# Optimization experiments

Hardware: AMD Instinct MI355X
Metric: run time of the kernel (lower is better)

The kernel has to match this reference:

```python
import jax, jax.numpy as jnp
import numpy as np

B, S, D0, H, K, C = 128, 64, 768, 256, 7, 3
EPS = 1e-12


def setup_inputs() -> dict:
    key = jax.random.key(0)
    ks = jax.random.split(key, 8)
    return {
        "premise": jax.random.normal(ks[0], (B, S, D0), jnp.float32),
        "hypothesis": jax.random.normal(ks[1], (B, S, D0), jnp.float32),
        "aW1": jax.random.normal(ks[2], (S, D0), jnp.float32) * 0.02,
        "conv1_w": jax.random.normal(ks[3], (D0, K, 2, H), jnp.float32) * 0.02,
        "conv1_b": jnp.full((H,), 1e-4, jnp.float32),
        "aW2": jax.random.normal(ks[4], (S, H), jnp.float32) * 0.02,
        "conv2_w": jax.random.normal(ks[5], (H, K, 2, H), jnp.float32) * 0.02,
        "conv2_b": jnp.full((H,), 1e-4, jnp.float32),
        "out_w": jax.random.normal(ks[6], (3, C), jnp.float32) * 0.1,
        "out_b": jnp.zeros((C,), jnp.float32),
    }


def _att_mat(x1, x2):
    # x1, x2: [B, d, W]; euclidean pairwise-distance attention 1/(1+||x1_i - x2_j||)
    n1 = jnp.sum(x1 * x1, axis=1)                       # [B, W]
    n2 = jnp.sum(x2 * x2, axis=1)                       # [B, W]
    dot = jnp.einsum('bdi,bdj->bij', x1, x2)            # [B, W, W]
    sq = jnp.maximum(n1[:, :, None] + n2[:, None, :] - 2.0 * dot, 0.0)
    return 1.0 / (1.0 + jnp.sqrt(sq + EPS))


def _cos_sim(v1, v2):
    n1 = jnp.sqrt(jnp.sum(v1 * v1, axis=1))
    n2 = jnp.sqrt(jnp.sum(v2 * v2, axis=1))
    return jnp.sum(v1 * v2, axis=1) / (n1 * n2 + EPS)


def _cnn_layer(x1, x2, aW, cw, cb):
    # x1, x2: [B, d, S]; aW: [S, d]; cw: [d, K, 2, H] (HWIO); cb: [H]
    att = _att_mat(x1, x2)                              # [B, S, S]
    # x1_a = (att @ aW)^T, x2_a = (att^T @ aW)^T  ->  [B, d, S]
    x1a = jnp.einsum('bij,jd->bdi', att, aW)
    x2a = jnp.einsum('bji,jd->bdi', att, aW)

    def conv(x, xa):
        xin = jnp.stack([x, xa], axis=-1)               # [B, d, S, 2] NHWC
        xin = jnp.pad(xin, ((0, 0), (0, 0), (K - 1, K - 1), (0, 0)))
        y = jax.lax.conv_general_dilated(
            xin, cw, window_strides=(1, 1), padding='VALID',
            dimension_numbers=('NHWC', 'HWIO', 'NHWC'))  # [B, 1, S+K-1, H]
        return jnp.transpose(jnp.tanh(y + cb)[:, 0], (0, 2, 1))  # [B, H, S+K-1]

    lc = conv(x1, x1a)
    rc = conv(x2, x2a)

    att2 = _att_mat(lc, rc)                             # [B, S+K-1, S+K-1]
    la = jnp.sum(att2, axis=2)                          # [B, S+K-1]
    ra = jnp.sum(att2, axis=1)                          # [B, S+K-1]

    def w_pool(x, a):
        # attention-weighted sliding-window sum of width K -> [B, H, S]
        w = x * a[:, None, :]
        return sum(w[:, :, j:j + S] for j in range(K))

    lwp = w_pool(lc, la)
    rwp = w_pool(rc, ra)
    lap = jnp.mean(lc, axis=2)                          # all-pool -> [B, H]
    rap = jnp.mean(rc, axis=2)
    return lwp, lap, rwp, rap


def _forward(premise, hypothesis, aW1, conv1_w, conv1_b, aW2, conv2_w, conv2_b,
             out_w, out_b):
    x1 = jnp.transpose(premise, (0, 2, 1))              # [B, D0, S]
    x2 = jnp.transpose(hypothesis, (0, 2, 1))
    LO0 = jnp.mean(x1, axis=2)                          # [B, D0]
    RO0 = jnp.mean(x2, axis=2)
    LI1, LO1, RI1, RO1 = _cnn_layer(x1, x2, aW1, conv1_w, conv1_b)
    _, LO2, _, RO2 = _cnn_layer(LI1, RI1, aW2, conv2_w, conv2_b)
    sims = jnp.stack(
        [_cos_sim(LO0, RO0), _cos_sim(LO1, RO1), _cos_sim(LO2, RO2)], axis=1)
    return sims @ out_w + out_b                         # logits [B, C]


def reference(premise, hypothesis, aW1, conv1_w, conv1_b, aW2, conv2_w,
              conv2_b, out_w, out_b):
    return _forward(premise, hypothesis, aW1, conv1_w, conv1_b, aW2, conv2_w,
                    conv2_b, out_w, out_b)
```

## Files before the change

### kernel.cpp

```cpp
#include <hip/hip_runtime.h>
#include <math.h>

typedef _Float16 f16;
typedef _Float16 half8 __attribute__((ext_vector_type(8)));
typedef _Float16 half4 __attribute__((ext_vector_type(4)));
typedef float floatx4 __attribute__((ext_vector_type(4)));

constexpr int B   = 128;
constexpr int S   = 64;
constexpr int D0  = 768;
constexpr int H   = 256;
constexpr int KW  = 7;
constexpr int NC  = 3;
constexpr int T70 = S + KW - 1;
constexpr float EPSF = 1e-12f;

__device__ __forceinline__ void gload16(const void* g, void* l) {
  __builtin_amdgcn_global_load_lds(
      (const __attribute__((address_space(1))) unsigned int*)g,
      (__attribute__((address_space(3))) unsigned int*)l, 16, 0, 0);
}

__global__ __launch_bounds__(256) void k_cvtmean(const float* __restrict__ in0,
                                                 const float* __restrict__ in1,
                                                 f16* __restrict__ oh0,
                                                 f16* __restrict__ oh1,
                                                 float* __restrict__ mn0,
                                                 float* __restrict__ mn1) {
  constexpr int D4 = D0 / 4;
  const int side = blockIdx.y;
  const float* __restrict__ in = side ? in1 : in0;
  f16* __restrict__ outh = side ? oh1 : oh0;
  float* __restrict__ mean = side ? mn1 : mn0;
  const int idx = blockIdx.x * 256 + threadIdx.x;
  const int b = idx / D4, f4 = idx % D4;
  const float4* __restrict__ src = reinterpret_cast<const float4*>(in) + (size_t)b * S * D4 + f4;
  half4* __restrict__ dst = reinterpret_cast<half4*>(outh) + (size_t)b * S * D4 + f4;
  float4 acc = {0.f, 0.f, 0.f, 0.f};
  for (int t = 0; t < S; ++t) {
    float4 v = src[(size_t)t * D4];
    acc.x += v.x; acc.y += v.y; acc.z += v.z; acc.w += v.w;
    half4 o = {(f16)v.x, (f16)v.y, (f16)v.z, (f16)v.w};
    dst[(size_t)t * D4] = o;
  }
  const float inv = 1.f / S;
  mean[(size_t)b * D0 + f4 * 4 + 0] = acc.x * inv;
  mean[(size_t)b * D0 + f4 * 4 + 1] = acc.y * inv;
  mean[(size_t)b * D0 + f4 * 4 + 2] = acc.z * inv;
  mean[(size_t)b * D0 + f4 * 4 + 3] = acc.w * inv;
}

__global__ __launch_bounds__(256) void k_trw_x(const float* __restrict__ cw,
                                               f16* __restrict__ Weff, int DPC, int Ktot) {
  __shared__ f16 tile[64][65];
  const int k = blockIdx.z;
  const int dd0 = blockIdx.x * 64, h0 = blockIdx.y * 64;
  const int tx = threadIdx.x & 63, ty = threadIdx.x >> 6;
#pragma unroll
  for (int i = 0; i < 64; i += 4) {
    int dd = dd0 + i + ty;
    tile[i + ty][tx] = (f16)cw[(size_t)((dd * KW + k) * 2 + 0) * H + h0 + tx];
  }
  __syncthreads();
  const int sbase = ((dd0 >> 6) * 7 + k) * 64;
#pragma unroll
  for (int i = 0; i < 64; i += 4) {
    int h = h0 + i + ty;
    int col = sbase + (((tx >> 3) ^ (h & 7)) << 3) + (tx & 7);
    Weff[(size_t)h * Ktot + col] = tile[tx][i + ty];
  }
}

template<int D>
__global__ __launch_bounds__(256) void k_vgemm(const float* __restrict__ aW,
                                               const float* __restrict__ cw,
                                               f16* __restrict__ Weff) {
  constexpr int NX7 = (D / 64) * 7;
  constexpr int KTOT = (NX7 + 7) * 64;
  __shared__ half8 As[64 * 4];
  __shared__ half8 Bs[64 * 4];
  const int kk = blockIdx.x;
  const int h0 = blockIdx.y * 64;
  const int tid = threadIdx.x;
  const int lane = tid & 63, wave = tid >> 6;
  const int wr = wave >> 1, wc = wave & 1;
  const int l15 = lane & 15, g = lane >> 4;

  floatx4 acc[2][2];
#pragma unroll
  for (int i = 0; i < 2; ++i)
#pragma unroll
    for (int j = 0; j < 2; ++j) acc[i][j] = (floatx4)0.f;

  for (int k0 = 0; k0 < D; k0 += 32) {
    __syncthreads();
    {
      const int r = tid >> 2, cch = tid & 3;
      const float4* s = reinterpret_cast<const float4*>(aW + (size_t)r * D + k0 + cch * 8);
      float4 v0 = s[0], v1 = s[1];
      half8 hv = {(f16)v0.x, (f16)v0.y, (f16)v0.z, (f16)v0.w,
                  (f16)v1.x, (f16)v1.y, (f16)v1.z, (f16)v1.w};
      As[r * 4 + (cch ^ ((r >> 1) & 3))] = hv;
      const int hrow = tid & 63, kc = tid >> 6;
      half8 bv;
#pragma unroll
      for (int e = 0; e < 8; ++e) {
        const int d = k0 + kc * 8 + e;
        bv[e] = (f16)cw[(size_t)((d * KW + kk) * 2 + 1) * H + h0 + hrow];
      }
      Bs[hrow * 4 + (kc ^ ((hrow >> 1) & 3))] = bv;
    }
    __syncthreads();
    half8 af[2], bf[2];
#pragma unroll
    for (int fi = 0; fi < 2; ++fi) {
      const int row = wr * 32 + fi * 16 + l15;
      af[fi] = As[row * 4 + (g ^ ((row >> 1) & 3))];
    }
#pragma unroll
    for (int fj = 0; fj < 2; ++fj) {
      const int row = wc * 32 + fj * 16 + l15;
      bf[fj] = Bs[row * 4 + (g ^ ((row >> 1) & 3))];
    }
#pragma unroll
    for (int fi = 0; fi < 2; ++fi)
#pragma unroll
      for (int fj = 0; fj < 2; ++fj)
        acc[fi][fj] = __builtin_amdgcn_mfma_f32_16x16x32_f16(af[fi], bf[fj], acc[fi][fj], 0, 0, 0);
  }
  const int base = (NX7 + kk) * 64;
#pragma unroll
  for (int fi = 0; fi < 2; ++fi)
#pragma unroll
    for (int fj = 0; fj < 2; ++fj)
#pragma unroll
      for (int r = 0; r < 4; ++r) {
        const int j = wr * 32 + fi * 16 + g * 4 + r;
        const int h = h0 + wc * 32 + fj * 16 + l15;
        const int col = base + (((j >> 3) ^ (h & 7)) << 3) + (j & 7);
        Weff[(size_t)h * KTOT + col] = (f16)acc[fi][fj][r];
      }
}

__global__ __launch_bounds__(256) void k_mean2(const f16* __restrict__ xa,
                                               const f16* __restrict__ xb,
                                               float* __restrict__ oa,
                                               float* __restrict__ ob) {
  const int side = blockIdx.y;
  const f16* __restrict__ x = side ? xb : xa;
  float* __restrict__ o = side ? ob : oa;
  int idx = blockIdx.x * 256 + threadIdx.x;
  if (idx >= B * H) return;
  int b = idx / H, f = idx % H;
  const f16* p = x + (size_t)b * T70 * H + f;
  float s = 0.f;
  for (int t = 0; t < T70; ++t) s += (float)p[(size_t)t * H];
  o[idx] = s * (1.f / T70);
}

template<int W, int WP, int D, bool SUMS>
__global__ __launch_bounds__(256) void k_att(const f16* __restrict__ X1,
                                             const f16* __restrict__ X2,
                                             float* __restrict__ la,
                                             float* __restrict__ ra) {
  constexpr int FR = WP / 32;
  __shared__ half8 As[WP * 4];
  __shared__ half8 Bs[WP * 4];
  __shared__ float n1s[WP], n2s[WP];
  __shared__ float att_s[SUMS ? WP * (WP + 1) : 1];

  const int b = blockIdx.x, tid = threadIdx.x;
  const int lane = tid & 63, wave = tid >> 6;
  const int wr = wave >> 1, wc = wave & 1;
  const int l15 = lane & 15, g = lane >> 4;
  const f16* __restrict__ x1 = X1 + (size_t)b * W * D;
  const f16* __restrict__ x2 = X2 + (size_t)b * W * D;

  floatx4 acc[FR][FR];
#pragma unroll
  for (int i = 0; i < FR; ++i)
#pragma unroll
    for (int j = 0; j < FR; ++j) acc[i][j] = (floatx4)0.f;
  float na1 = 0.f, na2 = 0.f;

  for (int k0 = 0; k0 < D; k0 += 32) {
    __syncthreads();
    for (int u = tid; u < WP * 4; u += 256) {
      const int r = u >> 2, c = u & 3;
      half8 v1 = (half8)(f16)0.f, v2 = (half8)(f16)0.f;
      if (r < W) {
        v1 = *reinterpret_cast<const half8*>(x1 + (size_t)r * D + k0 + c * 8);
        v2 = *reinterpret_cast<const half8*>(x2 + (size_t)r * D + k0 + c * 8);
      }
      const int p = r * 4 + (c ^ ((r >> 1) & 3));
      As[p] = v1;
      Bs[p] = v2;
    }
    __syncthreads();
    half8 af[FR], bf[FR];
#pragma unroll
    for (int fi = 0; fi < FR; ++fi) {
      const int row = wr * 16 * FR + fi * 16 + l15;
      af[fi] = As[row * 4 + (g ^ ((row >> 1) & 3))];
    }
#pragma unroll
    for (int fj = 0; fj < FR; ++fj) {
      const int row = wc * 16 * FR + fj * 16 + l15;
      bf[fj] = Bs[row * 4 + (g ^ ((row >> 1) & 3))];
    }
#pragma unroll
    for (int fi = 0; fi < FR; ++fi)
#pragma unroll
      for (int fj = 0; fj < FR; ++fj)
        acc[fi][fj] = __builtin_amdgcn_mfma_f32_16x16x32_f16(af[fi], bf[fj], acc[fi][fj], 0, 0, 0);
    if (tid < WP) {
      const int r = tid;
#pragma unroll
      for (int c = 0; c < 4; ++c) {
        half8 v = As[r * 4 + (c ^ ((r >> 1) & 3))];
#pragma unroll
        for (int e = 0; e < 8; ++e) { float f = (float)v[e]; na1 = fmaf(f, f, na1); }
      }
    } else if (tid >= 128 && tid < 128 + WP) {
      const int r = tid - 128;
#pragma unroll
      for (int c = 0; c < 4; ++c) {
        half8 v = Bs[r * 4 + (c ^ ((r >> 1) & 3))];
#pragma unroll
        for (int e = 0; e < 8; ++e) { float f = (float)v[e]; na2 = fmaf(f, f, na2); }
      }
    }
  }
  if (tid < WP) n1s[tid] = na1;
  if (tid >= 128 && tid < 128 + WP) n2s[tid - 128] = na2;
  __syncthreads();

#pragma unroll
  for (int fi = 0; fi < FR; ++fi)
#pragma unroll
    for (int fj = 0; fj < FR; ++fj)
#pragma unroll
      for (int r = 0; r < 4; ++r) {
        const int i = wr * 16 * FR + fi * 16 + g * 4 + r;
        const int j = wc * 16 * FR + fj * 16 + l15;
        if (i < W && j < W) {
          float sq = fmaxf(n1s[i] + n2s[j] - 2.f * acc[fi][fj][r], 0.f);
          const float v = 1.f / (1.f + sqrtf(sq + EPSF));
          if (SUMS) att_s[i * (WP + 1) + j] = v;
        }
      }
  if (SUMS) {
    __syncthreads();
    if (tid < W) {
      float sum = 0.f;
      for (int j = 0; j < W; ++j) sum += att_s[tid * (WP + 1) + j];
      la[b * W + tid] = sum;
    }
    if (tid >= 128 && tid < 128 + W) {
      const int j = tid - 128;
      float sum = 0.f;
      for (int i = 0; i < W; ++i) sum += att_s[i * (WP + 1) + j];
      ra[b * W + j] = sum;
    }
  }
}

template<int D>
__global__ __launch_bounds__(256) void k_attst(const f16* __restrict__ X1,
                                               const f16* __restrict__ X2,
                                               f16* __restrict__ attA,
                                               f16* __restrict__ attT) {
  __shared__ half8 As[64 * 4];
  __shared__ half8 Bs[64 * 4];
  __shared__ float n1s[64], n2s[64];
  __shared__ half8 atA[64 * 8];
  __shared__ half8 atT[64 * 8];

  const int b = blockIdx.x, tid = threadIdx.x;
  const int lane = tid & 63, wave = tid >> 6;
  const int wr = wave >> 1, wc = wave & 1;
  const int l15 = lane & 15, g = lane >> 4;
  const f16* __restrict__ x1 = X1 + (size_t)b * S * D;
  const f16* __restrict__ x2 = X2 + (size_t)b * S * D;

  floatx4 acc[2][2];
#pragma unroll
  for (int i = 0; i < 2; ++i)
#pragma unroll
    for (int j = 0; j < 2; ++j) acc[i][j] = (floatx4)0.f;
  float na1 = 0.f, na2 = 0.f;

  for (int k0 = 0; k0 < D; k0 += 32) {
    __syncthreads();
    {
      const int r = tid >> 2, c = tid & 3;
      const int p = r * 4 + (c ^ ((r >> 1) & 3));
      As[p] = *reinterpret_cast<const half8*>(x1 + (size_t)r * D + k0 + c * 8);
      Bs[p] = *reinterpret_cast<const half8*>(x2 + (size_t)r * D + k0 + c * 8);
    }
    __syncthreads();
    half8 af[2], bf[2];
#pragma unroll
    for (int fi = 0; fi < 2; ++fi) {
      const int row = wr * 32 + fi * 16 + l15;
      af[fi] = As[row * 4 + (g ^ ((row >> 1) & 3))];
    }
#pragma unroll
    for (int fj = 0; fj < 2; ++fj) {
      const int row = wc * 32 + fj * 16 + l15;
      bf[fj] = Bs[row * 4 + (g ^ ((row >> 1) & 3))];
    }
#pragma unroll
    for (int fi = 0; fi < 2; ++fi)
#pragma unroll
      for (int fj = 0; fj < 2; ++fj)
        acc[fi][fj] = __builtin_amdgcn_mfma_f32_16x16x32_f16(af[fi], bf[fj], acc[fi][fj], 0, 0, 0);
    if (tid < 64) {
      const int r = tid;
#pragma unroll
      for (int c = 0; c < 4; ++c) {
        half8 v = As[r * 4 + (c ^ ((r >> 1) & 3))];
#pragma unroll
        for (int e = 0; e < 8; ++e) { float f = (float)v[e]; na1 = fmaf(f, f, na1); }
      }
    } else if (tid >= 128 && tid < 192) {
      const int r = tid - 128;
#pragma unroll
      for (int c = 0; c < 4; ++c) {
        half8 v = Bs[r * 4 + (c ^ ((r >> 1) & 3))];
#pragma unroll
        for (int e = 0; e < 8; ++e) { float f = (float)v[e]; na2 = fmaf(f, f, na2); }
      }
    }
  }
  if (tid < 64) n1s[tid] = na1;
  if (tid >= 128 && tid < 192) n2s[tid - 128] = na2;
  __syncthreads();

  f16* atAe = reinterpret_cast<f16*>(atA);
  f16* atTe = reinterpret_cast<f16*>(atT);
#pragma unroll
  for (int fi = 0; fi < 2; ++fi)
#pragma unroll
    for (int fj = 0; fj < 2; ++fj)
#pragma unroll
      for (int r = 0; r < 4; ++r) {
        const int i = wr * 32 + fi * 16 + g * 4 + r;
        const int j = wc * 32 + fj * 16 + l15;
        float sq = fmaxf(n1s[i] + n2s[j] - 2.f * acc[fi][fj][r], 0.f);
        const f16 v = (f16)(1.f / (1.f + sqrtf(sq + EPSF)));
        atAe[(i * 8 + ((j >> 3) ^ (i & 7))) * 8 + (j & 7)] = v;
        atTe[(j * 8 + ((i >> 3) ^ (j & 7))) * 8 + (i & 7)] = v;
      }
  __syncthreads();
  half8* Ag = reinterpret_cast<half8*>(attA) + (size_t)b * 512;
  half8* Tg = reinterpret_cast<half8*>(attT) + (size_t)b * 512;
  for (int idx = tid; idx < 512; idx += 256) {
    const int i = idx >> 3, ch = idx & 7;
    Ag[idx] = atA[i * 8 + (ch ^ (i & 7))];
    Tg[idx] = atT[i * 8 + (ch ^ (i & 7))];
  }
}

template<int DPC>
__global__ __launch_bounds__(256) void k_conv(const f16* __restrict__ X0,
                                              const f16* __restrict__ X1v,
                                              const f16* __restrict__ At0,
                                              const f16* __restrict__ At1,
                                              const f16* __restrict__ Weff,
                                              const float* __restrict__ bias,
                                              f16* __restrict__ O16_0,
                                              f16* __restrict__ O16_1) {
  constexpr int NDQX = DPC / 64;
  constexpr int NX7 = NDQX * 7;
  constexpr int NSTEP = NX7 + 7;
  constexpr int KTOT = NSTEP * 64;
  __shared__ half8 Wl[70 * 8];
  __shared__ half8 B8[2][128 * 8];

  const int tid = threadIdx.x;
  const int bid = blockIdx.x;
  const int xcd = bid & 7, slot = bid >> 3;
  const int n0 = (xcd >> 2) * 128;
  const int w = slot * 4 + (xcd & 3);
  const int z = w & 1, mblk = w >> 1;
  const int m0 = mblk * 64;
  const f16* __restrict__ Xs  = z ? X1v : X0;
  const f16* __restrict__ Ats = z ? At1 : At0;
  f16* __restrict__ Out16 = z ? O16_1 : O16_0;

  const int lane = tid & 63, wave = tid >> 6;
  const int wr = wave >> 1, wc = wave & 1;
  const int l15 = lane & 15, g = lane >> 4;
  const int r0 = tid >> 3, c8 = tid & 7;

  int jr[3] = {r0, r0 + 32, 64 + r0};
  int aoffX[3], aoffA[3];
  bool aval[3];
#pragma unroll
  for (int p = 0; p < 3; ++p) {
    const int u = m0 - 6 + jr[p];
    const int uc = u < 0 ? 0 : u;
    const int bn = uc / T70;
    const int tl = uc - bn * T70;
    aval[p] = (u >= 0) && (tl < S);
    aoffX[p] = (bn * S + tl) * DPC + c8 * 8;
    aoffA[p] = (bn * 64 + tl) * 64 + c8 * 8;
  }
  const bool has2 = (r0 < 6);
  const int bchunk0 = wave * 64 + lane;
  const f16* __restrict__ bsrc = Weff + (size_t)n0 * KTOT;

  floatx4 acc[2][4];
#pragma unroll
  for (int i = 0; i < 2; ++i)
#pragma unroll
    for (int j = 0; j < 4; ++j) acc[i][j] = (floatx4)0.f;

  half8 rA[3];
  auto aLoad = [&](const f16* __restrict__ src, const int* aoff, int co) {
#pragma unroll
    for (int p = 0; p < 2; ++p)
      rA[p] = aval[p] ? *reinterpret_cast<const half8*>(src + aoff[p] + co)
                      : (half8)(f16)0.f;
    if (has2)
      rA[2] = aval[2] ? *reinterpret_cast<const half8*>(src + aoff[2] + co)
                      : (half8)(f16)0.f;
  };
  auto aWrite = [&]() {
#pragma unroll
    for (int p = 0; p < 2; ++p) {
      const int j = jr[p];
      Wl[j * 8 + (c8 ^ (j & 7))] = rA[p];
    }
    if (has2) {
      const int j = jr[2];
      Wl[j * 8 + (c8 ^ (j & 7))] = rA[2];
    }
  };
  auto bStage = [&](int buf, int ks) {
    const int o = ks * 64;
#pragma unroll
    for (int q = 0; q < 4; ++q) {
      const int chunk = q * 256 + bchunk0;
      const int r = chunk >> 3, cc = chunk & 7;
      gload16(bsrc + (size_t)r * KTOT + o + cc * 8, &B8[buf][q * 256 + wave * 64]);
    }
  };
  auto compute = [&](int ks) {
    const int k = (ks < NX7) ? (ks % 7) : (ks - NX7);
    const int buf = ks & 1;
    half8 af[2][2], bf[4][2];
#pragma unroll
    for (int i = 0; i < 2; ++i) {
      const int j = wr * 32 + i * 16 + l15 + k;
#pragma unroll
      for (int s = 0; s < 2; ++s)
        af[i][s] = Wl[j * 8 + ((s * 4 + g) ^ (j & 7))];
    }
#pragma unroll
    for (int jx = 0; jx < 4; ++jx) {
      const int row = wc * 64 + jx * 16 + l15;
#pragma unroll
      for (int s = 0; s < 2; ++s)
        bf[jx][s] = B8[buf][row * 8 + ((s * 4 + g) ^ (row & 7))];
    }
#pragma unroll
    for (int s = 0; s < 2; ++s)
#pragma unroll
      for (int i = 0; i < 2; ++i)
#pragma unroll
        for (int jx = 0; jx < 4; ++jx)
          acc[i][jx] = __builtin_amdgcn_mfma_f32_16x16x32_f16(af[i][s], bf[jx][s], acc[i][jx], 0, 0, 0);
  };

  bStage(0, 0);
  aLoad(Xs, aoffX, 0);
  aWrite();
  __syncthreads();

  for (int ks = 0; ks < NSTEP; ++ks) {
    const int nxt = ks + 1;
    const bool more = nxt < NSTEP;
    if (more) {
      bStage(nxt & 1, nxt);
      if (ks % 7 == 5) {
        const int wnd = ks / 7 + 1;
        if (wnd < NDQX) aLoad(Xs, aoffX, wnd * 64);
        else if (wnd == NDQX) aLoad(Ats, aoffA, 0);
      }
    }
    compute(ks);
    if (more && (nxt % 7 == 0)) { __syncthreads(); aWrite(); }
    __syncthreads();
  }

#pragma unroll
  for (int i = 0; i < 2; ++i) {
    const int mr = m0 + wr * 32 + i * 16 + g * 4;
#pragma unroll
    for (int jx = 0; jx < 4; ++jx) {
      const int h = n0 + wc * 64 + jx * 16 + l15;
      const float bv = bias[h];
#pragma unroll
      for (int r = 0; r < 4; ++r)
        Out16[(size_t)(mr + r) * H + h] = (f16)tanhf(acc[i][jx][r] + bv);
    }
  }
}

__global__ __launch_bounds__(256) void k_powl(const f16* __restrict__ lcTh,
                                              const f16* __restrict__ rcTh,
                                              const float* __restrict__ la,
                                              const float* __restrict__ ra,
                                              float* __restrict__ LO1,
                                              float* __restrict__ RO1,
                                              f16* __restrict__ LI1h,
                                              f16* __restrict__ RI1h) {
  const int b = blockIdx.x, side = blockIdx.y;
  const f16* __restrict__ xc = (side ? rcTh : lcTh) + (size_t)b * T70 * H;
  const float* __restrict__ av = (side ? ra : la) + (size_t)b * T70;
  float* __restrict__ LO = side ? RO1 : LO1;
  f16* __restrict__ LI = (side ? RI1h : LI1h) + (size_t)b * S * H;
  __shared__ float a_s[T70];
  __shared__ f16 wv[T70][H];
  const int h = threadIdx.x;
  if (h < T70) a_s[h] = av[h];
  __syncthreads();
  float sum = 0.f;
  for (int t = 0; t < T70; ++t) {
    const float v = (float)xc[(size_t)t * H + h];
    sum += v;
    wv[t][h] = (f16)(v * a_s[t]);
  }
  LO[(size_t)b * H + h] = sum * (1.f / T70);
  __syncthreads();
  for (int s = 0; s < S; ++s) {
    float acc = 0.f;
#pragma unroll
    for (int j = 0; j < KW; ++j) acc += (float)wv[s + j][h];
    LI[(size_t)s * H + h] = (f16)acc;
  }
}

__global__ __launch_bounds__(256) void k_final(const float* __restrict__ LO0,
                                               const float* __restrict__ RO0,
                                               const float* __restrict__ LO1,
                                               const float* __restrict__ RO1,
                                               const float* __restrict__ LO2,
                                               const float* __restrict__ RO2,
                                               const float* __restrict__ out_w,
                                               const float* __restrict__ out_b,
                                               float* __restrict__ out) {
  const int b = blockIdx.x;
  const int tid = threadIdx.x;
  __shared__ float red[3][4];
  __shared__ float sims[3];
  const float* Ls[3] = {LO0 + (size_t)b * D0, LO1 + (size_t)b * H, LO2 + (size_t)b * H};
  const float* Rs[3] = {RO0 + (size_t)b * D0, RO1 + (size_t)b * H, RO2 + (size_t)b * H};
  const int dims[3] = {D0, H, H};
#pragma unroll
  for (int p = 0; p < 3; ++p) {
    float dot = 0.f, q1 = 0.f, q2 = 0.f;
    for (int i = tid; i < dims[p]; i += 256) {
      const float v1 = Ls[p][i], v2 = Rs[p][i];
      dot = fmaf(v1, v2, dot);
      q1  = fmaf(v1, v1, q1);
      q2  = fmaf(v2, v2, q2);
    }
#pragma unroll
    for (int off = 32; off > 0; off >>= 1) {
      dot += __shfl_down(dot, off);
      q1  += __shfl_down(q1, off);
      q2  += __shfl_down(q2, off);
    }
    if ((tid & 63) == 0) { red[0][tid >> 6] = dot; red[1][tid >> 6] = q1; red[2][tid >> 6] = q2; }
    __syncthreads();
    if (tid == 0) {
      float d = red[0][0] + red[0][1] + red[0][2] + red[0][3];
      float a = red[1][0] + red[1][1] + red[1][2] + red[1][3];
      float c = red[2][0] + red[2][1] + red[2][2] + red[2][3];
      sims[p] = d / (sqrtf(a) * sqrtf(c) + EPSF);
    }
    __syncthreads();
  }
  if (tid < NC) {
    float v = out_b[tid];
#pragma unroll
    for (int k = 0; k < 3; ++k) v = fmaf(sims[k], out_w[k * NC + tid], v);
    out[b * NC + tid] = v;
  }
}

extern "C" void kernel_launch(void* const* d_in, const int* in_sizes, int n_in,
                              void* d_out, int out_size, void* d_ws, size_t ws_size,
                              hipStream_t stream) {
  const float* premise    = (const float*)d_in[0];
  const float* hypothesis = (const float*)d_in[1];
  const float* aW1        = (const float*)d_in[2];
  const float* conv1_w    = (const float*)d_in[3];
  const float* conv1_b    = (const float*)d_in[4];
  const float* aW2        = (const float*)d_in[5];
  const float* conv2_w    = (const float*)d_in[6];
  const float* conv2_b    = (const float*)d_in[7];
  const float* out_w      = (const float*)d_in[8];
  const float* out_b      = (const float*)d_in[9];
  float* out = (float*)d_out;

  constexpr int KTOT1 = ((D0 / 64) * 7 + 7) * 64;
  constexpr int KTOT2 = ((H  / 64) * 7 + 7) * 64;

  char* ws = (char*)d_ws;
  size_t off = 0;
  auto alloc = [&](size_t bytes) {
    void* p = ws + off;
    off += (bytes + 255) & ~(size_t)255;
    return p;
  };
  f16*   Weff1 = (f16*)alloc((size_t)H * KTOT1 * 2);
  f16*   Weff2 = (f16*)alloc((size_t)H * KTOT2 * 2);
  f16*   Xh    = (f16*)alloc((size_t)B * S * D0 * 2);
  f16*   Yh    = (f16*)alloc((size_t)B * S * D0 * 2);
  f16*   attA  = (f16*)alloc((size_t)B * S * S * 2);
  f16*   attT  = (f16*)alloc((size_t)B * S * S * 2);
  f16*   LI1h  = (f16*)alloc((size_t)B * S * H * 2);
  f16*   RI1h  = (f16*)alloc((size_t)B * S * H * 2);
  f16*   lcTh  = (f16*)alloc((size_t)B * T70 * H * 2);
  f16*   rcTh  = (f16*)alloc((size_t)B * T70 * H * 2);
  float* LO0   = (float*)alloc((size_t)B * D0 * 4);
  float* RO0   = (float*)alloc((size_t)B * D0 * 4);
  float* LO1   = (float*)alloc((size_t)B * H * 4);
  float* RO1   = (float*)alloc((size_t)B * H * 4);
  float* LO2   = (float*)alloc((size_t)B * H * 4);
  float* RO2   = (float*)alloc((size_t)B * H * 4);
  float* la    = (float*)alloc((size_t)B * T70 * 4);
  float* ra    = (float*)alloc((size_t)B * T70 * 4);

  k_cvtmean<<<dim3(B * (D0 / 4) / 256, 2), 256, 0, stream>>>(premise, hypothesis, Xh, Yh, LO0, RO0);
  k_trw_x<<<dim3(D0 / 64, H / 64, 7), 256, 0, stream>>>(conv1_w, Weff1, D0, KTOT1);
  k_trw_x<<<dim3(H / 64,  H / 64, 7), 256, 0, stream>>>(conv2_w, Weff2, H, KTOT2);
  k_vgemm<D0><<<dim3(7, H / 64), 256, 0, stream>>>(aW1, conv1_w, Weff1);
  k_vgemm<H ><<<dim3(7, H / 64), 256, 0, stream>>>(aW2, conv2_w, Weff2);
  k_attst<D0><<<B, 256, 0, stream>>>(Xh, Yh, attA, attT);
  k_conv<D0><<<560, 256, 0, stream>>>(Xh, Yh, attA, attT, Weff1, conv1_b, lcTh, rcTh);
  k_att<T70, 96, H, true><<<B, 256, 0, stream>>>(lcTh, rcTh, la, ra);
  k_powl<<<dim3(B, 2), 256, 0, stream>>>(lcTh, rcTh, la, ra, LO1, RO1, LI1h, RI1h);
  k_attst<H><<<B, 256, 0, stream>>>(LI1h, RI1h, attA, attT);
  k_conv<H><<<560, 256, 0, stream>>>(LI1h, RI1h, attA, attT, Weff2, conv2_b, lcTh, rcTh);
  k_mean2<<<dim3((B * H + 255) / 256, 2), 256, 0, stream>>>(lcTh, rcTh, LO2, RO2);
  k_final<<<B, 256, 0, stream>>>(LO0, RO0, LO1, RO1, LO2, RO2, out_w, out_b, out);
}
```

Before: 226.2 us.

## Fuse weight-prep and pooling kernels, triple-buffer conv pipeline with raw barriers

The four weight-preparation launches become one kernel, k_wprep, that picks its role from the block index. The attention-sum and weighted-pool kernels are merged into k_pool, one block per batch that handles both sides. The final mean of the second layer's conv outputs moves into k_final. The conv GEMM now triple-buffers the B operand and double-buffers the A window, and uses explicit vmcnt waits, s_barrier and setprio around the MFMAs instead of __syncthreads. This cuts launch count and intermediate round trips, and overlaps loads with MFMA work. The cost is more LDS per conv block, hand-tuned wait counts that could be fragile, and k_pool running half as many blocks as the old pooling kernel.

```diff
diff --git a/kernel.cpp b/kernel.cpp
--- a/kernel.cpp
+++ b/kernel.cpp
@@ -14,6 +14,8 @@
 constexpr int NC  = 3;
 constexpr int T70 = S + KW - 1;
 constexpr float EPSF = 1e-12f;
+constexpr int KTOT1 = ((D0 / 64) * 7 + 7) * 64;
+constexpr int KTOT2 = ((H  / 64) * 7 + 7) * 64;
 
 __device__ __forceinline__ void gload16(const void* g, void* l) {
   __builtin_amdgcn_global_load_lds(
@@ -50,11 +52,14 @@
   mean[(size_t)b * D0 + f4 * 4 + 3] = acc.w * inv;
 }
 
-__global__ __launch_bounds__(256) void k_trw_x(const float* __restrict__ cw,
-                                               f16* __restrict__ Weff, int DPC, int Ktot) {
-  __shared__ f16 tile[64][65];
-  const int k = blockIdx.z;
-  const int dd0 = blockIdx.x * 64, h0 = blockIdx.y * 64;
+__device__ __forceinline__ void trw_x_dev(const float* __restrict__ cw,
+                                          f16* __restrict__ Weff,
+                                          int DPC, int Ktot, int t,
+                                          f16 (*tile)[65]) {
+  const int nb = DPC / 64;
+  const int k = t / (nb * 4);
+  const int rem = t % (nb * 4);
+  const int h0 = (rem / nb) * 64, dd0 = (rem % nb) * 64;
   const int tx = threadIdx.x & 63, ty = threadIdx.x >> 6;
 #pragma unroll
   for (int i = 0; i < 64; i += 4) {
@@ -71,16 +76,13 @@
   }
 }
 
-template<int D>
-__global__ __launch_bounds__(256) void k_vgemm(const float* __restrict__ aW,
-                                               const float* __restrict__ cw,
-                                               f16* __restrict__ Weff) {
-  constexpr int NX7 = (D / 64) * 7;
-  constexpr int KTOT = (NX7 + 7) * 64;
-  __shared__ half8 As[64 * 4];
-  __shared__ half8 Bs[64 * 4];
-  const int kk = blockIdx.x;
-  const int h0 = blockIdx.y * 64;
+__device__ __forceinline__ void vgemm_dev(const float* __restrict__ aW,
+                                          const float* __restrict__ cw,
+                                          f16* __restrict__ Weff,
+                                          int D, int Ktot, int t,
+                                          half8* As, half8* Bs) {
+  const int kk = t % 7;
+  const int h0 = (t / 7) * 64;
   const int tid = threadIdx.x;
   const int lane = tid & 63, wave = tid >> 6;
   const int wr = wave >> 1, wc = wave & 1;
@@ -128,7 +130,7 @@
       for (int fj = 0; fj < 2; ++fj)
         acc[fi][fj] = __builtin_amdgcn_mfma_f32_16x16x32_f16(af[fi], bf[fj], acc[fi][fj], 0, 0, 0);
   }
-  const int base = (NX7 + kk) * 64;
+  const int base = ((D / 64) * 7 + kk) * 64;
 #pragma unroll
   for (int fi = 0; fi < 2; ++fi)
 #pragma unroll
@@ -138,131 +140,24 @@
         const int j = wr * 32 + fi * 16 + g * 4 + r;
         const int h = h0 + wc * 32 + fj * 16 + l15;
         const int col = base + (((j >> 3) ^ (h & 7)) << 3) + (j & 7);
-        Weff[(size_t)h * KTOT + col] = (f16)acc[fi][fj][r];
-      }
-}
-
-__global__ __launch_bounds__(256) void k_mean2(const f16* __restrict__ xa,
-                                               const f16* __restrict__ xb,
-                                               float* __restrict__ oa,
-                                               float* __restrict__ ob) {
-  const int side = blockIdx.y;
-  const f16* __restrict__ x = side ? xb : xa;
-  float* __restrict__ o = side ? ob : oa;
-  int idx = blockIdx.x * 256 + threadIdx.x;
-  if (idx >= B * H) return;
-  int b = idx / H, f = idx % H;
-  const f16* p = x + (size_t)b * T70 * H + f;
-  float s = 0.f;
-  for (int t = 0; t < T70; ++t) s += (float)p[(size_t)t * H];
-  o[idx] = s * (1.f / T70);
-}
-
-template<int W, int WP, int D, bool SUMS>
-__global__ __launch_bounds__(256) void k_att(const f16* __restrict__ X1,
-                                             const f16* __restrict__ X2,
-                                             float* __restrict__ la,
-                                             float* __restrict__ ra) {
-  constexpr int FR = WP / 32;
-  __shared__ half8 As[WP * 4];
-  __shared__ half8 Bs[WP * 4];
-  __shared__ float n1s[WP], n2s[WP];
-  __shared__ float att_s[SUMS ? WP * (WP + 1) : 1];
-
-  const int b = blockIdx.x, tid = threadIdx.x;
-  const int lane = tid & 63, wave = tid >> 6;
-  const int wr = wave >> 1, wc = wave & 1;
-  const int l15 = lane & 15, g = lane >> 4;
-  const f16* __restrict__ x1 = X1 + (size_t)b * W * D;
-  const f16* __restrict__ x2 = X2 + (size_t)b * W * D;
-
-  floatx4 acc[FR][FR];
-#pragma unroll
-  for (int i = 0; i < FR; ++i)
-#pragma unroll
-    for (int j = 0; j < FR; ++j) acc[i][j] = (floatx4)0.f;
-  float na1 = 0.f, na2 = 0.f;
-
-  for (int k0 = 0; k0 < D; k0 += 32) {
-    __syncthreads();
-    for (int u = tid; u < WP * 4; u += 256) {
-      const int r = u >> 2, c = u & 3;
-      half8 v1 = (half8)(f16)0.f, v2 = (half8)(f16)0.f;
-      if (r < W) {
-        v1 = *reinterpret_cast<const half8*>(x1 + (size_t)r * D + k0 + c * 8);
-        v2 = *reinterpret_cast<const half8*>(x2 + (size_t)r * D + k0 + c * 8);
-      }
-      const int p = r * 4 + (c ^ ((r >> 1) & 3));
-      As[p] = v1;
-      Bs[p] = v2;
-    }
-    __syncthreads();
-    half8 af[FR], bf[FR];
-#pragma unroll
-    for (int fi = 0; fi < FR; ++fi) {
-      const int row = wr * 16 * FR + fi * 16 + l15;
-      af[fi] = As[row * 4 + (g ^ ((row >> 1) & 3))];
-    }
-#pragma unroll
-    for (int fj = 0; fj < FR; ++fj) {
-      const int row = wc * 16 * FR + fj * 16 + l15;
-      bf[fj] = Bs[row * 4 + (g ^ ((row >> 1) & 3))];
-    }
-#pragma unroll
-    for (int fi = 0; fi < FR; ++fi)
-#pragma unroll
-      for (int fj = 0; fj < FR; ++fj)
-        acc[fi][fj] = __builtin_amdgcn_mfma_f32_16x16x32_f16(af[fi], bf[fj], acc[fi][fj], 0, 0, 0);
-    if (tid < WP) {
-      const int r = tid;
-#pragma unroll
-      for (int c = 0; c < 4; ++c) {
-        half8 v = As[r * 4 + (c ^ ((r >> 1) & 3))];
-#pragma unroll
-        for (int e = 0; e < 8; ++e) { float f = (float)v[e]; na1 = fmaf(f, f, na1); }
-      }
-    } else if (tid >= 128 && tid < 128 + WP) {
-      const int r = tid - 128;
-#pragma unroll
-      for (int c = 0; c < 4; ++c) {
-        half8 v = Bs[r * 4 + (c ^ ((r >> 1) & 3))];
-#pragma unroll
-        for (int e = 0; e < 8; ++e) { float f = (float)v[e]; na2 = fmaf(f, f, na2); }
-      }
-    }
-  }
-  if (tid < WP) n1s[tid] = na1;
-  if (tid >= 128 && tid < 128 + WP) n2s[tid - 128] = na2;
-  __syncthreads();
-
-#pragma unroll
-  for (int fi = 0; fi < FR; ++fi)
-#pragma unroll
-    for (int fj = 0; fj < FR; ++fj)
-#pragma unroll
-      for (int r = 0; r < 4; ++r) {
-        const int i = wr * 16 * FR + fi * 16 + g * 4 + r;
-        const int j = wc * 16 * FR + fj * 16 + l15;
-        if (i < W && j < W) {
-          float sq = fmaxf(n1s[i] + n2s[j] - 2.f * acc[fi][fj][r], 0.f);
-          const float v = 1.f / (1.f + sqrtf(sq + EPSF));
-          if (SUMS) att_s[i * (WP + 1) + j] = v;
-        }
-      }
-  if (SUMS) {
-    __syncthreads();
-    if (tid < W) {
-      float sum = 0.f;
-      for (int j = 0; j < W; ++j) sum += att_s[tid * (WP + 1) + j];
-      la[b * W + tid] = sum;
-    }
-    if (tid >= 128 && tid < 128 + W) {
-      const int j = tid - 128;
-      float sum = 0.f;
-      for (int i = 0; i < W; ++i) sum += att_s[i * (WP + 1) + j];
-      ra[b * W + j] = sum;
-    }
-  }
+        Weff[(size_t)h * Ktot + col] = (f16)acc[fi][fj][r];
+      }
+}
+
+__global__ __launch_bounds__(256) void k_wprep(const float* __restrict__ cw1,
+                                               const float* __restrict__ aW1,
+                                               f16* __restrict__ Weff1,
+                                               const float* __restrict__ cw2,
+                                               const float* __restrict__ aW2,
+                                               f16* __restrict__ Weff2) {
+  __shared__ f16 tile[64][65];
+  __shared__ half8 As[64 * 4];
+  __shared__ half8 Bs[64 * 4];
+  const int bid = blockIdx.x;
+  if (bid < 336)        trw_x_dev(cw1, Weff1, D0, KTOT1, bid, tile);
+  else if (bid < 364)   vgemm_dev(aW1, cw1, Weff1, D0, KTOT1, bid - 336, As, Bs);
+  else if (bid < 476)   trw_x_dev(cw2, Weff2, H, KTOT2, bid - 364, tile);
+  else                  vgemm_dev(aW2, cw2, Weff2, H, KTOT2, bid - 476, As, Bs);
 }
 
 template<int D>
@@ -375,8 +270,8 @@
   constexpr int NX7 = NDQX * 7;
   constexpr int NSTEP = NX7 + 7;
   constexpr int KTOT = NSTEP * 64;
-  __shared__ half8 Wl[70 * 8];
-  __shared__ half8 B8[2][128 * 8];
+  __shared__ half8 Wl[2][70 * 8];
+  __shared__ half8 B8[3][128 * 8];
 
   const int tid = threadIdx.x;
   const int bid = blockIdx.x;
@@ -427,15 +322,15 @@
       rA[2] = aval[2] ? *reinterpret_cast<const half8*>(src + aoff[2] + co)
                       : (half8)(f16)0.f;
   };
-  auto aWrite = [&]() {
+  auto aWrite = [&](int bufA) {
 #pragma unroll
     for (int p = 0; p < 2; ++p) {
       const int j = jr[p];
-      Wl[j * 8 + (c8 ^ (j & 7))] = rA[p];
+      Wl[bufA][j * 8 + (c8 ^ (j & 7))] = rA[p];
     }
     if (has2) {
       const int j = jr[2];
-      Wl[j * 8 + (c8 ^ (j & 7))] = rA[2];
+      Wl[bufA][j * 8 + (c8 ^ (j & 7))] = rA[2];
     }
   };
   auto bStage = [&](int buf, int ks) {
@@ -448,15 +343,16 @@
     }
   };
   auto compute = [&](int ks) {
-    const int k = (ks < NX7) ? (ks % 7) : (ks - NX7);
-    const int buf = ks & 1;
+    const int k = ks % 7;
+    const int buf = ks % 3;
+    const int bufA = (ks / 7) & 1;
     half8 af[2][2], bf[4][2];
 #pragma unroll
     for (int i = 0; i < 2; ++i) {
       const int j = wr * 32 + i * 16 + l15 + k;
 #pragma unroll
       for (int s = 0; s < 2; ++s)
-        af[i][s] = Wl[j * 8 + ((s * 4 + g) ^ (j & 7))];
+        af[i][s] = Wl[bufA][j * 8 + ((s * 4 + g) ^ (j & 7))];
     }
 #pragma unroll
     for (int jx = 0; jx < 4; ++jx) {
@@ -465,6 +361,7 @@
       for (int s = 0; s < 2; ++s)
         bf[jx][s] = B8[buf][row * 8 + ((s * 4 + g) ^ (row & 7))];
     }
+    __builtin_amdgcn_s_setprio(1);
 #pragma unroll
     for (int s = 0; s < 2; ++s)
 #pragma unroll
@@ -472,27 +369,38 @@
 #pragma unroll
         for (int jx = 0; jx < 4; ++jx)
           acc[i][jx] = __builtin_amdgcn_mfma_f32_16x16x32_f16(af[i][s], bf[jx][s], acc[i][jx], 0, 0, 0);
+    __builtin_amdgcn_s_setprio(0);
   };
 
   bStage(0, 0);
   aLoad(Xs, aoffX, 0);
-  aWrite();
-  __syncthreads();
+  bStage(1, 1);
+  aWrite(0);
+  asm volatile("s_waitcnt vmcnt(4) lgkmcnt(0)" ::: "memory");
+  __builtin_amdgcn_s_barrier();
+  __builtin_amdgcn_sched_barrier(0);
 
   for (int ks = 0; ks < NSTEP; ++ks) {
-    const int nxt = ks + 1;
-    const bool more = nxt < NSTEP;
-    if (more) {
-      bStage(nxt & 1, nxt);
-      if (ks % 7 == 5) {
-        const int wnd = ks / 7 + 1;
-        if (wnd < NDQX) aLoad(Xs, aoffX, wnd * 64);
-        else if (wnd == NDQX) aLoad(Ats, aoffA, 0);
-      }
+    const int nxt = ks + 1, nn = ks + 2;
+    if (nn < NSTEP) bStage(nn % 3, nn);
+    if ((ks % 7) == 5) {
+      const int wnd = ks / 7 + 1;
+      if (wnd < NDQX) aLoad(Xs, aoffX, wnd * 64);
+      else if (wnd == NDQX) aLoad(Ats, aoffA, 0);
     }
     compute(ks);
-    if (more && (nxt % 7 == 0)) { __syncthreads(); aWrite(); }
-    __syncthreads();
+    const bool awr = (nxt < NSTEP) && ((nxt % 7) == 0);
+    if (awr) aWrite((nxt / 7) & 1);
+    if (nxt < NSTEP) {
+      if (nn < NSTEP) {
+        if (awr) asm volatile("s_waitcnt vmcnt(4) lgkmcnt(0)" ::: "memory");
+        else     asm volatile("s_waitcnt vmcnt(4)" ::: "memory");
+      } else {
+        asm volatile("s_waitcnt vmcnt(0) lgkmcnt(0)" ::: "memory");
+      }
+      __builtin_amdgcn_s_barrier();
+      __builtin_amdgcn_sched_barrier(0);
+    }
   }
 
 #pragma unroll
@@ -509,37 +417,136 @@
   }
 }
 
-__global__ __launch_bounds__(256) void k_powl(const f16* __restrict__ lcTh,
+__global__ __launch_bounds__(256) void k_pool(const f16* __restrict__ lcTh,
                                               const f16* __restrict__ rcTh,
-                                              const float* __restrict__ la,
-                                              const float* __restrict__ ra,
                                               float* __restrict__ LO1,
                                               float* __restrict__ RO1,
                                               f16* __restrict__ LI1h,
                                               f16* __restrict__ RI1h) {
-  const int b = blockIdx.x, side = blockIdx.y;
-  const f16* __restrict__ xc = (side ? rcTh : lcTh) + (size_t)b * T70 * H;
-  const float* __restrict__ av = (side ? ra : la) + (size_t)b * T70;
-  float* __restrict__ LO = side ? RO1 : LO1;
-  f16* __restrict__ LI = (side ? RI1h : LI1h) + (size_t)b * S * H;
-  __shared__ float a_s[T70];
-  __shared__ f16 wv[T70][H];
-  const int h = threadIdx.x;
-  if (h < T70) a_s[h] = av[h];
+  constexpr int W = T70, WP = 96, D = H;
+  constexpr int FR = WP / 32;
+  __shared__ half8 As[WP * 4];
+  __shared__ half8 Bs[WP * 4];
+  __shared__ float n1s[WP], n2s[WP];
+  __shared__ float att_s[WP * (WP + 1)];
+  __shared__ float la_s[W], ra_s[W];
+
+  const int b = blockIdx.x, tid = threadIdx.x;
+  const int lane = tid & 63, wave = tid >> 6;
+  const int wr = wave >> 1, wc = wave & 1;
+  const int l15 = lane & 15, g = lane >> 4;
+  const f16* __restrict__ x1 = lcTh + (size_t)b * W * D;
+  const f16* __restrict__ x2 = rcTh + (size_t)b * W * D;
+
+  floatx4 acc[FR][FR];
+#pragma unroll
+  for (int i = 0; i < FR; ++i)
+#pragma unroll
+    for (int j = 0; j < FR; ++j) acc[i][j] = (floatx4)0.f;
+  float na1 = 0.f, na2 = 0.f;
+
+  for (int k0 = 0; k0 < D; k0 += 32) {
+    __syncthreads();
+    for (int u = tid; u < WP * 4; u += 256) {
+      const int r = u >> 2, c = u & 3;
+      half8 v1 = (half8)(f16)0.f, v2 = (half8)(f16)0.f;
+      if (r < W) {
+        v1 = *reinterpret_cast<const half8*>(x1 + (size_t)r * D + k0 + c * 8);
+        v2 = *reinterpret_cast<const half8*>(x2 + (size_t)r * D + k0 + c * 8);
+      }
+      const int p = r * 4 + (c ^ ((r >> 1) & 3));
+      As[p] = v1;
+      Bs[p] = v2;
+    }
+    __syncthreads();
+    half8 af[FR], bf[FR];
+#pragma unroll
+    for (int fi = 0; fi < FR; ++fi) {
+      const int row = wr * 16 * FR + fi * 16 + l15;
+      af[fi] = As[row * 4 + (g ^ ((row >> 1) & 3))];
+    }
+#pragma unroll
+    for (int fj = 0; fj < FR; ++fj) {
+      const int row = wc * 16 * FR + fj * 16 + l15;
+      bf[fj] = Bs[row * 4 + (g ^ ((row >> 1) & 3))];
+    }
+#pragma unroll
+    for (int fi = 0; fi < FR; ++fi)
+#pragma unroll
+      for (int fj = 0; fj < FR; ++fj)
+        acc[fi][fj] = __builtin_amdgcn_mfma_f32_16x16x32_f16(af[fi], bf[fj], acc[fi][fj], 0, 0, 0);
+    if (tid < WP) {
+      const int r = tid;
+#pragma unroll
+      for (int c = 0; c < 4; ++c) {
+        half8 v = As[r * 4 + (c ^ ((r >> 1) & 3))];
+#pragma unroll
+        for (int e = 0; e < 8; ++e) { float f = (float)v[e]; na1 = fmaf(f, f, na1); }
+      }
+    } else if (tid >= 128 && tid < 128 + WP) {
+      const int r = tid - 128;
+#pragma unroll
+      for (int c = 0; c < 4; ++c) {
+        half8 v = Bs[r * 4 + (c ^ ((r >> 1) & 3))];
+#pragma unroll
+        for (int e = 0; e < 8; ++e) { float f = (float)v[e]; na2 = fmaf(f, f, na2); }
+      }
+    }
+  }
+  if (tid < WP) n1s[tid] = na1;
+  if (tid >= 128 && tid < 128 + WP) n2s[tid - 128] = na2;
   __syncthreads();
-  float sum = 0.f;
-  for (int t = 0; t < T70; ++t) {
-    const float v = (float)xc[(size_t)t * H + h];
-    sum += v;
-    wv[t][h] = (f16)(v * a_s[t]);
-  }
-  LO[(size_t)b * H + h] = sum * (1.f / T70);
+
+#pragma unroll
+  for (int fi = 0; fi < FR; ++fi)
+#pragma unroll
+    for (int fj = 0; fj < FR; ++fj)
+#pragma unroll
+      for (int r = 0; r < 4; ++r) {
+        const int i = wr * 16 * FR + fi * 16 + g * 4 + r;
+        const int j = wc * 16 * FR + fj * 16 + l15;
+        if (i < W && j < W) {
+          float sq = fmaxf(n1s[i] + n2s[j] - 2.f * acc[fi][fj][r], 0.f);
+          att_s[i * (WP + 1) + j] = 1.f / (1.f + sqrtf(sq + EPSF));
+        }
+      }
   __syncthreads();
-  for (int s = 0; s < S; ++s) {
-    float acc = 0.f;
-#pragma unroll
-    for (int j = 0; j < KW; ++j) acc += (float)wv[s + j][h];
-    LI[(size_t)s * H + h] = (f16)acc;
+  if (tid < W) {
+    float sum = 0.f;
+    for (int j = 0; j < W; ++j) sum += att_s[tid * (WP + 1) + j];
+    la_s[tid] = sum;
+  }
+  if (tid >= 128 && tid < 128 + W) {
+    const int j = tid - 128;
+    float sum = 0.f;
+    for (int i = 0; i < W; ++i) sum += att_s[i * (WP + 1) + j];
+    ra_s[j] = sum;
+  }
+  __syncthreads();
+
+  f16 (*wv)[H] = reinterpret_cast<f16(*)[H]>(att_s);
+  const int h = tid;
+#pragma unroll
+  for (int side = 0; side < 2; ++side) {
+    const f16* __restrict__ xc = (side ? rcTh : lcTh) + (size_t)b * T70 * H;
+    const float* __restrict__ av = side ? ra_s : la_s;
+    float* __restrict__ LO = side ? RO1 : LO1;
+    f16* __restrict__ LI = (side ? RI1h : LI1h) + (size_t)b * S * H;
+    __syncthreads();
+    float sum = 0.f;
+    for (int t = 0; t < T70; ++t) {
+      const float v = (float)xc[(size_t)t * H + h];
+      sum += v;
+      wv[t][h] = (f16)(v * av[t]);
+    }
+    LO[(size_t)b * H + h] = sum * (1.f / T70);
+    __syncthreads();
+    for (int s = 0; s < S; ++s) {
+      float a = 0.f;
+#pragma unroll
+      for (int j = 0; j < KW; ++j) a += (float)wv[s + j][h];
+      LI[(size_t)s * H + h] = (f16)a;
+    }
   }
 }
 
@@ -547,8 +554,8 @@
                                                const float* __restrict__ RO0,
                                                const float* __restrict__ LO1,
                                                const float* __restrict__ RO1,
-                                               const float* __restrict__ LO2,
-                                               const float* __restrict__ RO2,
+                                               const f16* __restrict__ lcTh,
+                                               const f16* __restrict__ rcTh,
                                                const float* __restrict__ out_w,
                                                const float* __restrict__ out_b,
                                                float* __restrict__ out) {
@@ -556,17 +563,35 @@
   const int tid = threadIdx.x;
   __shared__ float red[3][4];
   __shared__ float sims[3];
-  const float* Ls[3] = {LO0 + (size_t)b * D0, LO1 + (size_t)b * H, LO2 + (size_t)b * H};
-  const float* Rs[3] = {RO0 + (size_t)b * D0, RO1 + (size_t)b * H, RO2 + (size_t)b * H};
-  const int dims[3] = {D0, H, H};
+
+  float lo2 = 0.f, ro2 = 0.f;
+  {
+    const f16* lp = lcTh + (size_t)b * T70 * H + tid;
+    const f16* rp = rcTh + (size_t)b * T70 * H + tid;
+    for (int t = 0; t < T70; ++t) {
+      lo2 += (float)lp[(size_t)t * H];
+      ro2 += (float)rp[(size_t)t * H];
+    }
+    lo2 *= (1.f / T70);
+    ro2 *= (1.f / T70);
+  }
+
+  const float* Ls[2] = {LO0 + (size_t)b * D0, LO1 + (size_t)b * H};
+  const float* Rs[2] = {RO0 + (size_t)b * D0, RO1 + (size_t)b * H};
+  const int dims[2] = {D0, H};
 #pragma unroll
   for (int p = 0; p < 3; ++p) {
-    float dot = 0.f, q1 = 0.f, q2 = 0.f;
-    for (int i = tid; i < dims[p]; i += 256) {
-      const float v1 = Ls[p][i], v2 = Rs[p][i];
-      dot = fmaf(v1, v2, dot);
-      q1  = fmaf(v1, v1, q1);
-      q2  = fmaf(v2, v2, q2);
+    float dot, q1, q2;
+    if (p < 2) {
+      dot = 0.f; q1 = 0.f; q2 = 0.f;
+      for (int i = tid; i < dims[p]; i += 256) {
+        const float v1 = Ls[p][i], v2 = Rs[p][i];
+        dot = fmaf(v1, v2, dot);
+        q1  = fmaf(v1, v1, q1);
+        q2  = fmaf(v2, v2, q2);
+      }
+    } else {
+      dot = lo2 * ro2; q1 = lo2 * lo2; q2 = ro2 * ro2;
     }
 #pragma unroll
     for (int off = 32; off > 0; off >>= 1) {
@@ -606,9 +631,6 @@
   const float* out_w      = (const float*)d_in[8];
   const float* out_b      = (const float*)d_in[9];
   float* out = (float*)d_out;
-
-  constexpr int KTOT1 = ((D0 / 64) * 7 + 7) * 64;
-  constexpr int KTOT2 = ((H  / 64) * 7 + 7) * 64;
 
   char* ws = (char*)d_ws;
   size_t off = 0;
@@ -631,22 +653,13 @@
   float* RO0   = (float*)alloc((size_t)B * D0 * 4);
   float* LO1   = (float*)alloc((size_t)B * H * 4);
   float* RO1   = (float*)alloc((size_t)B * H * 4);
-  float* LO2   = (float*)alloc((size_t)B * H * 4);
-  float* RO2   = (float*)alloc((size_t)B * H * 4);
-  float* la    = (float*)alloc((size_t)B * T70 * 4);
-  float* ra    = (float*)alloc((size_t)B * T70 * 4);
 
   k_cvtmean<<<dim3(B * (D0 / 4) / 256, 2), 256, 0, stream>>>(premise, hypothesis, Xh, Yh, LO0, RO0);
-  k_trw_x<<<dim3(D0 / 64, H / 64, 7), 256, 0, stream>>>(conv1_w, Weff1, D0, KTOT1);
-  k_trw_x<<<dim3(H / 64,  H / 64, 7), 256, 0, stream>>>(conv2_w, Weff2, H, KTOT2);
-  k_vgemm<D0><<<dim3(7, H / 64), 256, 0, stream>>>(aW1, conv1_w, Weff1);
-  k_vgemm<H ><<<dim3(7, H / 64), 256, 0, stream>>>(aW2, conv2_w, Weff2);
+  k_wprep<<<504, 256, 0, stream>>>(conv1_w, aW1, Weff1, conv2_w, aW2, Weff2);
   k_attst<D0><<<B, 256, 0, stream>>>(Xh, Yh, attA, attT);
   k_conv<D0><<<560, 256, 0, stream>>>(Xh, Yh, attA, attT, Weff1, conv1_b, lcTh, rcTh);
-  k_att<T70, 96, H, true><<<B, 256, 0, stream>>>(lcTh, rcTh, la, ra);
-  k_powl<<<dim3(B, 2), 256, 0, stream>>>(lcTh, rcTh, la, ra, LO1, RO1, LI1h, RI1h);
+  k_pool<<<B, 256, 0, stream>>>(lcTh, rcTh, LO1, RO1, LI1h, RI1h);
   k_attst<H><<<B, 256, 0, stream>>>(LI1h, RI1h, attA, attT);
   k_conv<H><<<560, 256, 0, stream>>>(LI1h, RI1h, attA, attT, Weff2, conv2_b, lcTh, rcTh);
-  k_mean2<<<dim3((B * H + 255) / 256, 2), 256, 0, stream>>>(lcTh, rcTh, LO2, RO2);
-  k_final<<<B, 256, 0, stream>>>(LO0, RO0, LO1, RO1, LO2, RO2, out_w, out_b, out);
-}
+  k_final<<<B, 256, 0, stream>>>(LO0, RO0, LO1, RO1, lcTh, rcTh, out_w, out_b, out);
+}
```

After: 299.9 us. 1.33x slower.
